# Kernel tuning notes

Measured on AMD Instinct MI355X. Metric: run time of the kernel, lower is better.

Reference implementation:

```python
import jax, jax.numpy as jnp
import numpy as np
import math

EMB, HID, SEQ, BATCH, VOCAB, LAYERS = 512, 1024, 128, 64, 10000, 2


def setup_inputs() -> dict:
    key = jax.random.key(0)
    ks = jax.random.split(key, 8)
    bnd = math.sqrt(1.0 / HID)
    return {
        "inputs": jax.random.randint(ks[0], (SEQ, BATCH), 0, VOCAB),
        "hidden": jnp.zeros((LAYERS, BATCH, HID), jnp.float32),
        "emb": jax.random.uniform(ks[1], (VOCAB, EMB), jnp.float32, -0.1, 0.1),
        "W_x0": jax.random.uniform(ks[2], (EMB, HID), jnp.float32, -bnd, bnd),
        "W_x1": jax.random.uniform(ks[3], (HID, HID), jnp.float32, -bnd, bnd),
        "W_h": jax.random.uniform(ks[4], (LAYERS, HID, HID), jnp.float32, -bnd, bnd),
        "b_h": jax.random.uniform(ks[5], (LAYERS, HID), jnp.float32, -bnd, bnd),
        "W_out": jax.random.uniform(ks[6], (HID, VOCAB), jnp.float32, -0.1, 0.1),
        "b_out": jnp.zeros((VOCAB,), jnp.float32),
    }


def reference(inputs, hidden, emb, W_x0, W_x1, W_h, b_h, W_out, b_out):
    # Stacked vanilla RNN over time; dropout is identity (dp_keep_prob=1.0).
    scale = jnp.asarray(math.sqrt(EMB), jnp.float32)  # WordEmbedding * sqrt(n_units)

    def step(h, tok):
        # h: (L, B, H); tok: (B,)
        x = emb[tok] * scale                                   # (B, E)
        h0 = jnp.tanh(x @ W_x0 + h[0] @ W_h[0] + b_h[0])       # (B, H)
        h1 = jnp.tanh(h0 @ W_x1 + h[1] @ W_h[1] + b_h[1])      # (B, H)
        logits_t = h1 @ W_out + b_out                          # (B, V)
        return jnp.stack([h0, h1]), logits_t

    final_hidden, logits = jax.lax.scan(step, hidden, inputs)
    return logits, final_hidden
```

## Files before the change

kernel.cpp:

```cpp
#include <hip/hip_runtime.h>
#include <math.h>


typedef unsigned short u16;
typedef unsigned long long u64;
typedef __bf16 bf16x8 __attribute__((ext_vector_type(8)));
typedef float  f32x4  __attribute__((ext_vector_type(4)));
typedef unsigned int u32x4 __attribute__((ext_vector_type(4)));
typedef u16 u16x8 __attribute__((ext_vector_type(8)));

#define SEQ_ 128
#define B_   64
#define E_   512
#define H_   1024
#define V_   10000
#define VP_  10112
#define ROWS_ (SEQ_*B_)
#define BH_  (B_*H_)
#define LOGITS_ 81920000
#define NWG_ 192

__device__ __forceinline__ u16 f2bf(float f) {
  unsigned u = __builtin_bit_cast(unsigned, f);
  u += 0x7fffu + ((u >> 16) & 1u);
  return (u16)(u >> 16);
}
__device__ __forceinline__ float bf2f(u16 h) {
  unsigned u = ((unsigned)h) << 16;
  return __builtin_bit_cast(float, u);
}
__device__ __forceinline__ void st64(void* p, u64 v) {
  __hip_atomic_store((u64*)p, v, __ATOMIC_RELAXED, __HIP_MEMORY_SCOPE_AGENT);
}
__device__ __forceinline__ u64 pk64(float a, float b) {
  return (u64)__builtin_bit_cast(unsigned, a) |
         ((u64)__builtin_bit_cast(unsigned, b) << 32);
}


__global__ __launch_bounds__(256)
void transpose_split(const float* __restrict__ in, u16* __restrict__ outHi,
                     u16* __restrict__ outLo, int K, int N, int NP)
{
  __shared__ float tile[32][33];
  const int n0 = blockIdx.x * 32, k0 = blockIdx.y * 32;
  const int x = threadIdx.x & 31;
  const int y = threadIdx.x >> 5;
  (void)NP;
#pragma unroll
  for (int i = 0; i < 4; ++i) {
    const int r = y * 4 + i;
    const int n = n0 + x;
    tile[r][x] = (n < N) ? in[(size_t)(k0 + r) * N + n] : 0.f;
  }
  __syncthreads();
#pragma unroll
  for (int i = 0; i < 4; ++i) {
    const int r = y * 4 + i;
    const int n = n0 + r;
    const int k = k0 + x;
    const float v = tile[x][r];
    const u16 hb = f2bf(v);
    outHi[(size_t)n * K + k] = hb;
    if (outLo) outLo[(size_t)n * K + k] = f2bf(v - bf2f(hb));
  }
}

__global__ __launch_bounds__(256)
void gather_x(const int* __restrict__ toks, const float* __restrict__ emb,
              u16* __restrict__ XBhi, u16* __restrict__ XBlo)
{
  const int tid = blockIdx.x * 256 + threadIdx.x;
  const int row = tid >> 6;
  const int c8 = (tid & 63) * 8;
  const int tok = toks[row];
  const float* e = emb + (size_t)tok * E_ + c8;
  u16x8 hv, lv;
#pragma unroll
  for (int j = 0; j < 8; ++j) {
    float f = e[j] * 22.627416997969522f;
    u16 hb = f2bf(f);
    hv[j] = hb;
    lv[j] = f2bf(f - bf2f(hb));
  }
  *(u16x8*)(XBhi + (size_t)row * E_ + c8) = hv;
  *(u16x8*)(XBlo + (size_t)row * E_ + c8) = lv;
}

__global__ __launch_bounds__(256)
void hid_cast(const float* __restrict__ h, u16* H0hi, u16* H0lo, u16* H1hi, u16* H1lo)
{
  const int tid = blockIdx.x * 256 + threadIdx.x;
  float v0 = h[tid], v1 = h[BH_ + tid];
  u16 a = f2bf(v0); H0hi[tid] = a; H0lo[tid] = f2bf(v0 - bf2f(a));
  u16 b = f2bf(v1); H1hi[tid] = b; H1lo[tid] = f2bf(v1 - bf2f(b));
}

template<int NPASS>
__global__ __launch_bounds__(256)
void gemm_bf16(const u16* __restrict__ Ahi, const u16* __restrict__ Alo,
               const u16* __restrict__ Bhi, const u16* __restrict__ Blo,
               const float* __restrict__ bias, float* __restrict__ C,
               int K, int Nreal, int ldc, int nbx, int nby)
{
  constexpr int LDT = 40;
  __shared__ u16 lds[(NPASS == 3 ? 4 : 2) * 128 * LDT];
  u16* As  = lds;
  u16* Bs  = lds + 128 * LDT;
  u16* As2 = (NPASS == 3) ? (lds + 2 * 128 * LDT) : lds;
  u16* Bs2 = (NPASS == 3) ? (lds + 3 * 128 * LDT) : lds;

  const int S = 8;
  int bid  = blockIdx.x;
  int scol = bid / (S * nby);
  int rem  = bid - scol * (S * nby);
  int w    = nbx - scol * S; if (w > S) w = S;
  int bx   = scol * S + rem % w;
  int by   = rem / w;
  const int m0 = by * 128, n0 = bx * 128;

  const int tid  = threadIdx.x;
  const int wave = tid >> 6, lane = tid & 63;
  const int wm = (wave & 1) * 64, wn = (wave >> 1) * 64;
  const int lrow = lane & 15, lk = (lane >> 4) * 8;

  f32x4 acc[4][4] = {};

  const int kTiles = K >> 5;
  for (int kt = 0; kt < kTiles; ++kt) {
    const int k0 = kt << 5;
    __syncthreads();
#pragma unroll
    for (int c = tid; c < 512; c += 256) {
      const int row = c >> 2, kq = c & 3;
      const int l = row * LDT + kq * 8;
      *(u32x4*)(As + l) = *(const u32x4*)(Ahi + (size_t)(m0 + row) * K + k0 + kq * 8);
      *(u32x4*)(Bs + l) = *(const u32x4*)(Bhi + (size_t)(n0 + row) * K + k0 + kq * 8);
      if constexpr (NPASS == 3) {
        *(u32x4*)(As2 + l) = *(const u32x4*)(Alo + (size_t)(m0 + row) * K + k0 + kq * 8);
        *(u32x4*)(Bs2 + l) = *(const u32x4*)(Blo + (size_t)(n0 + row) * K + k0 + kq * 8);
      }
    }
    __syncthreads();
    bf16x8 a[4], b[4];
#pragma unroll
    for (int i = 0; i < 4; ++i) {
      a[i] = *(const bf16x8*)(As + (wm + i * 16 + lrow) * LDT + lk);
      b[i] = *(const bf16x8*)(Bs + (wn + i * 16 + lrow) * LDT + lk);
    }
    if constexpr (NPASS == 3) {
      bf16x8 a2[4], b2[4];
#pragma unroll
      for (int i = 0; i < 4; ++i) {
        a2[i] = *(const bf16x8*)(As2 + (wm + i * 16 + lrow) * LDT + lk);
        b2[i] = *(const bf16x8*)(Bs2 + (wn + i * 16 + lrow) * LDT + lk);
      }
#pragma unroll
      for (int mi = 0; mi < 4; ++mi)
#pragma unroll
        for (int ni = 0; ni < 4; ++ni) {
          acc[mi][ni] = __builtin_amdgcn_mfma_f32_16x16x32_bf16(a[mi],  b[ni],  acc[mi][ni], 0, 0, 0);
          acc[mi][ni] = __builtin_amdgcn_mfma_f32_16x16x32_bf16(a[mi],  b2[ni], acc[mi][ni], 0, 0, 0);
          acc[mi][ni] = __builtin_amdgcn_mfma_f32_16x16x32_bf16(a2[mi], b[ni],  acc[mi][ni], 0, 0, 0);
        }
    } else {
#pragma unroll
      for (int mi = 0; mi < 4; ++mi)
#pragma unroll
        for (int ni = 0; ni < 4; ++ni)
          acc[mi][ni] = __builtin_amdgcn_mfma_f32_16x16x32_bf16(a[mi], b[ni], acc[mi][ni], 0, 0, 0);
    }
  }
#pragma unroll
  for (int mi = 0; mi < 4; ++mi)
#pragma unroll
    for (int ni = 0; ni < 4; ++ni)
#pragma unroll
      for (int r = 0; r < 4; ++r) {
        const int row = m0 + wm + mi * 16 + (lane >> 4) * 4 + r;
        const int col = n0 + wn + ni * 16 + lrow;
        if (col < Nreal) {
          float v = acc[mi][ni][r];
          if (bias) v += bias[col];
          C[(size_t)row * ldc + col] = v;
        }
      }
}

__device__ __forceinline__ void gbar192(unsigned* flags, unsigned my)
{
  asm volatile("s_waitcnt vmcnt(0)" ::: "memory");
  __syncthreads();
  if (threadIdx.x == 0)
    __hip_atomic_store(flags + blockIdx.x * 16u, my, __ATOMIC_RELAXED,
                       __HIP_MEMORY_SCOPE_AGENT);
  if (threadIdx.x < 64) {
    const int l = threadIdx.x;
    bool ok0 = false, ok1 = false, ok2 = false;
    for (;;) {
      if (!ok0) ok0 = __hip_atomic_load(flags + l * 16,         __ATOMIC_RELAXED, __HIP_MEMORY_SCOPE_AGENT) >= my;
      if (!ok1) ok1 = __hip_atomic_load(flags + (l + 64) * 16,  __ATOMIC_RELAXED, __HIP_MEMORY_SCOPE_AGENT) >= my;
      if (!ok2) ok2 = __hip_atomic_load(flags + (l + 128) * 16, __ATOMIC_RELAXED, __HIP_MEMORY_SCOPE_AGENT) >= my;
      if (__all(ok0 && ok1 && ok2)) break;
      __builtin_amdgcn_s_sleep(2);
    }
  }
  __syncthreads();
}

__global__ __launch_bounds__(256, 1)
void recur_fused(const u16* __restrict__ Wh0h, const u16* __restrict__ Wh0l,
                 const u16* __restrict__ Wx1h, const u16* __restrict__ Wx1l,
                 const u16* __restrict__ Wh1h, const u16* __restrict__ Wh1l,
                 const float* __restrict__ XP0, const float* __restrict__ b1,
                 float* __restrict__ Pbuf,
                 u16* __restrict__ H0hi, u16* __restrict__ H0lo,
                 u16* __restrict__ H1hi, u16* __restrict__ H1lo,
                 float* __restrict__ final0, float* __restrict__ final1,
                 unsigned* __restrict__ flags)
{
  __shared__ u16 bsm[2 * 32 * 1024];

  const int wg   = blockIdx.x;
  const int role = (wg < 64) ? 0 : (wg < 128) ? 1 : 2;
  const int idx  = wg & 63;
  const int bg   = idx >> 5, cg = idx & 31;

  const u16* Bhi = (role == 0) ? Wh0h : (role == 1) ? Wx1h : Wh1h;
  const u16* Blo = (role == 0) ? Wh0l : (role == 1) ? Wx1l : Wh1l;

  const int tid  = threadIdx.x;
  const int wv   = tid >> 6, lane = tid & 63;
  const int wbg  = wv >> 1, wcg = wv & 1;
  const int lb   = lane & 15;
  const int lk8  = (lane >> 4) * 8;

  for (int c = tid; c < 8192; c += 256) {
    const int p   = c >> 12;
    const int cc  = c & 4095;
    const int col = cc >> 7;
    const int k8  = (cc & 127) * 8;
    u32x4 v = *(const u32x4*)((p ? Blo : Bhi) + (size_t)(cg * 32 + col) * H_ + k8);
    *(u32x4*)(bsm + p * 32768 + col * 1024 + (k8 ^ ((col & 7) << 3))) = v;
  }
  __syncthreads();

  const int batch = bg * 32 + wbg * 16 + lb;
  const int c0    = cg * 32 + wcg * 16 + (lk8 >> 1);
  const int colL  = wcg * 16 + lb;
  const int xorv  = (colL & 7) << 3;
  const u16* bsp  = bsm + colL * 1024;
  const size_t aoff = (size_t)batch * H_ + lk8;

  for (int i = 0; i < 130; ++i) {
    bool active; int t;
    if (role == 0)      { active = (i < 128);           t = i;     }
    else if (role == 1) { active = (i >= 1 && i < 129); t = i - 1; }
    else                { active = (i >= 2);            t = i - 2; }

    if (active) {
      const u16 *Ahi, *Alo;
      const float* initp;
      if (role == 0) {
        Ahi = H0hi + (size_t)t * BH_;  Alo = H0lo + (size_t)t * BH_;
        initp = XP0 + (size_t)t * BH_ + (size_t)batch * H_ + c0;
      } else if (role == 1) {
        Ahi = H0hi + (size_t)(t + 1) * BH_;  Alo = H0lo + (size_t)(t + 1) * BH_;
        initp = b1 + c0;
      } else {
        Ahi = H1hi + (size_t)t * BH_;  Alo = H1lo + (size_t)t * BH_;
        initp = Pbuf + (size_t)t * BH_ + (size_t)batch * H_ + c0;
      }

      f32x4 acc0 = *(const f32x4*)initp;
      f32x4 acc1 = {0.f, 0.f, 0.f, 0.f};
#pragma unroll
      for (int kc = 0; kc < 32; ++kc) {
        bf16x8 ah = *(const bf16x8*)(Ahi + aoff + kc * 32);
        bf16x8 al = *(const bf16x8*)(Alo + aoff + kc * 32);
        bf16x8 bh = *(const bf16x8*)(bsp + ((kc * 32 + lk8) ^ xorv));
        bf16x8 bl = *(const bf16x8*)(bsp + 32768 + ((kc * 32 + lk8) ^ xorv));
        if (kc & 1) {
          acc1 = __builtin_amdgcn_mfma_f32_16x16x32_bf16(bh, ah, acc1, 0, 0, 0);
          acc1 = __builtin_amdgcn_mfma_f32_16x16x32_bf16(bl, ah, acc1, 0, 0, 0);
          acc1 = __builtin_amdgcn_mfma_f32_16x16x32_bf16(bh, al, acc1, 0, 0, 0);
        } else {
          acc0 = __builtin_amdgcn_mfma_f32_16x16x32_bf16(bh, ah, acc0, 0, 0, 0);
          acc0 = __builtin_amdgcn_mfma_f32_16x16x32_bf16(bl, ah, acc0, 0, 0, 0);
          acc0 = __builtin_amdgcn_mfma_f32_16x16x32_bf16(bh, al, acc0, 0, 0, 0);
        }
      }
      acc0 = acc0 + acc1;

      if (role == 1) {
        float* op = Pbuf + (size_t)t * BH_ + (size_t)batch * H_ + c0;
        st64(op,     pk64(acc0[0], acc0[1]));
        st64(op + 2, pk64(acc0[2], acc0[3]));
      } else {
        float hv[4];
        u64 whi = 0, wlo = 0;
#pragma unroll
        for (int r = 0; r < 4; ++r) {
          float v = tanhf(acc0[r]);
          u16 hb = f2bf(v);
          u16 lo = f2bf(v - bf2f(hb));
          whi |= (u64)hb << (16 * r);
          wlo |= (u64)lo << (16 * r);
          hv[r] = v;
        }
        u16* OH = (role == 0 ? H0hi : H1hi) + (size_t)(t + 1) * BH_ + (size_t)batch * H_ + c0;
        u16* OL = (role == 0 ? H0lo : H1lo) + (size_t)(t + 1) * BH_ + (size_t)batch * H_ + c0;
        st64(OH, whi);
        st64(OL, wlo);
        if (t == SEQ_ - 1) {
          float* fp = (role == 0 ? final0 : final1) + (size_t)batch * H_ + c0;
          st64(fp,     pk64(hv[0], hv[1]));
          st64(fp + 2, pk64(hv[2], hv[3]));
        }
      }
    }
    if (i < 129) gbar192(flags, (unsigned)(i + 1));
  }
}

extern "C" void kernel_launch(void* const* d_in, const int* in_sizes, int n_in,
                              void* d_out, int out_size, void* d_ws, size_t ws_size,
                              hipStream_t stream)
{
  (void)in_sizes; (void)n_in; (void)out_size; (void)ws_size;
  const int*   toks = (const int*)d_in[0];
  const float* hid0 = (const float*)d_in[1];
  const float* emb  = (const float*)d_in[2];
  const float* Wx0  = (const float*)d_in[3];
  const float* Wx1  = (const float*)d_in[4];
  const float* Wh   = (const float*)d_in[5];
  const float* bh   = (const float*)d_in[6];
  const float* Wout = (const float*)d_in[7];
  const float* bout = (const float*)d_in[8];
  float* out = (float*)d_out;

  char* ws = (char*)d_ws;
  size_t off = 0;
  auto alloc = [&](size_t bytes) -> void* {
    void* p = ws + off;
    off += (bytes + 255) & ~(size_t)255;
    return p;
  };
  unsigned* flags = (unsigned*)alloc(16384);
  u16* XBhi  = (u16*)alloc((size_t)ROWS_ * E_ * 2);
  u16* XBlo  = (u16*)alloc((size_t)ROWS_ * E_ * 2);
  u16* Wx0Th = (u16*)alloc((size_t)H_ * E_ * 2);
  u16* Wx0Tl = (u16*)alloc((size_t)H_ * E_ * 2);
  u16* Wx1Th = (u16*)alloc((size_t)H_ * H_ * 2);
  u16* Wx1Tl = (u16*)alloc((size_t)H_ * H_ * 2);
  u16* Wh0Th = (u16*)alloc((size_t)H_ * H_ * 2);
  u16* Wh0Tl = (u16*)alloc((size_t)H_ * H_ * 2);
  u16* Wh1Th = (u16*)alloc((size_t)H_ * H_ * 2);
  u16* Wh1Tl = (u16*)alloc((size_t)H_ * H_ * 2);
  u16* WoutT = (u16*)alloc((size_t)VP_ * H_ * 2);
  float* XP0 = (float*)alloc((size_t)ROWS_ * H_ * 4);
  float* Pbuf= (float*)alloc((size_t)SEQ_ * BH_ * 4);
  u16* H0hi  = (u16*)alloc((size_t)(SEQ_ + 1) * BH_ * 2);
  u16* H0lo  = (u16*)alloc((size_t)(SEQ_ + 1) * BH_ * 2);
  u16* H1hi  = (u16*)alloc((size_t)(SEQ_ + 1) * BH_ * 2);
  u16* H1lo  = (u16*)alloc((size_t)(SEQ_ + 1) * BH_ * 2);

  hipMemsetAsync(flags, 0, 16384, stream);
  transpose_split<<<dim3(H_ / 32, E_ / 32), 256, 0, stream>>>(Wx0, Wx0Th, Wx0Tl, E_, H_, H_);
  transpose_split<<<dim3(H_ / 32, H_ / 32), 256, 0, stream>>>(Wx1, Wx1Th, Wx1Tl, H_, H_, H_);
  transpose_split<<<dim3(H_ / 32, H_ / 32), 256, 0, stream>>>(Wh,           Wh0Th, Wh0Tl, H_, H_, H_);
  transpose_split<<<dim3(H_ / 32, H_ / 32), 256, 0, stream>>>(Wh + H_ * H_, Wh1Th, Wh1Tl, H_, H_, H_);
  transpose_split<<<dim3(VP_ / 32, H_ / 32), 256, 0, stream>>>(Wout, WoutT, nullptr, H_, V_, VP_);
  gather_x<<<ROWS_ * E_ / 8 / 256, 256, 0, stream>>>(toks, emb, XBhi, XBlo);
  hid_cast<<<BH_ / 256, 256, 0, stream>>>(hid0, H0hi, H0lo, H1hi, H1lo);

  gemm_bf16<3><<<8 * 64, 256, 0, stream>>>(XBhi, XBlo, Wx0Th, Wx0Tl, bh, XP0,
                                           E_, H_, H_, 8, 64);
  recur_fused<<<NWG_, 256, 0, stream>>>(Wh0Th, Wh0Tl, Wx1Th, Wx1Tl, Wh1Th, Wh1Tl,
                                        XP0, bh + H_, Pbuf,
                                        H0hi, H0lo, H1hi, H1lo,
                                        out + LOGITS_, out + LOGITS_ + BH_, flags);
  gemm_bf16<1><<<79 * 64, 256, 0, stream>>>(H1hi + BH_, nullptr, WoutT, nullptr,
                                            bout, out, H_, V_, V_, 79, 64);
}
```

Measured before the change: 1.741 ms.

## Replace global grid barrier with per-wave dataflow flags in recurrent kernel

The single 192-workgroup barrier per step is replaced by fine-grained per-wave, per-timestep, per-batch-group flags. Each role now waits only on the specific producers it depends on: layer0 on itself, the Wx1 projection on layer0, and layer1 on itself and the projection. This lets the pipeline stages drift relative to each other and removes __syncthreads from the step loop. It also swaps tanhf for an exp/rcp-based fast tanh, which may lose some accuracy near saturation and uses a much larger flag array that must be zeroed each launch.

```diff
diff --git a/kernel.cpp b/kernel.cpp
--- a/kernel.cpp
+++ b/kernel.cpp
@@ -19,6 +19,7 @@
 #define BH_  (B_*H_)
 #define LOGITS_ 81920000
 #define NWG_ 192
+#define FPS_ (129*128)
 
 __device__ __forceinline__ u16 f2bf(float f) {
   unsigned u = __builtin_bit_cast(unsigned, f);
@@ -35,6 +36,10 @@
 __device__ __forceinline__ u64 pk64(float a, float b) {
   return (u64)__builtin_bit_cast(unsigned, a) |
          ((u64)__builtin_bit_cast(unsigned, b) << 32);
+}
+__device__ __forceinline__ float tanh_fast(float x) {
+  float e = __expf(2.0f * x);
+  return 1.0f - 2.0f * __builtin_amdgcn_rcpf(e + 1.0f);
 }
 
 
@@ -187,29 +192,51 @@
       }
 }
 
-__device__ __forceinline__ void gbar192(unsigned* flags, unsigned my)
+__device__ __forceinline__ void pollW(const unsigned* f)
+{
+  const int l = threadIdx.x & 63;
+  for (;;) {
+    unsigned a = __hip_atomic_load(f + l,      __ATOMIC_RELAXED, __HIP_MEMORY_SCOPE_AGENT);
+    unsigned b = __hip_atomic_load(f + l + 64, __ATOMIC_RELAXED, __HIP_MEMORY_SCOPE_AGENT);
+    if (__all((a != 0) & (b != 0))) break;
+    __builtin_amdgcn_s_sleep(1);
+  }
+  asm volatile("" ::: "memory");
+}
+__device__ __forceinline__ void publish(unsigned* f)
 {
   asm volatile("s_waitcnt vmcnt(0)" ::: "memory");
-  __syncthreads();
-  if (threadIdx.x == 0)
-    __hip_atomic_store(flags + blockIdx.x * 16u, my, __ATOMIC_RELAXED,
-                       __HIP_MEMORY_SCOPE_AGENT);
-  if (threadIdx.x < 64) {
-    const int l = threadIdx.x;
-    bool ok0 = false, ok1 = false, ok2 = false;
-    for (;;) {
-      if (!ok0) ok0 = __hip_atomic_load(flags + l * 16,         __ATOMIC_RELAXED, __HIP_MEMORY_SCOPE_AGENT) >= my;
-      if (!ok1) ok1 = __hip_atomic_load(flags + (l + 64) * 16,  __ATOMIC_RELAXED, __HIP_MEMORY_SCOPE_AGENT) >= my;
-      if (!ok2) ok2 = __hip_atomic_load(flags + (l + 128) * 16, __ATOMIC_RELAXED, __HIP_MEMORY_SCOPE_AGENT) >= my;
-      if (__all(ok0 && ok1 && ok2)) break;
-      __builtin_amdgcn_s_sleep(2);
-    }
-  }
-  __syncthreads();
+  if ((threadIdx.x & 63) == 0)
+    __hip_atomic_store(f, 1u, __ATOMIC_RELAXED, __HIP_MEMORY_SCOPE_AGENT);
+}
+
+__device__ __forceinline__ f32x4 gemm96(const u16* __restrict__ Ahi,
+                                        const u16* __restrict__ Alo,
+                                        const u16* bsp, int xorv, int lk8,
+                                        size_t aoff, f32x4 acc0)
+{
+  f32x4 acc1 = {0.f, 0.f, 0.f, 0.f};
+#pragma unroll
+  for (int kc = 0; kc < 32; ++kc) {
+    bf16x8 ah = *(const bf16x8*)(Ahi + aoff + kc * 32);
+    bf16x8 al = *(const bf16x8*)(Alo + aoff + kc * 32);
+    bf16x8 bh = *(const bf16x8*)(bsp + ((kc * 32 + lk8) ^ xorv));
+    bf16x8 bl = *(const bf16x8*)(bsp + 32768 + ((kc * 32 + lk8) ^ xorv));
+    if (kc & 1) {
+      acc1 = __builtin_amdgcn_mfma_f32_16x16x32_bf16(bh, ah, acc1, 0, 0, 0);
+      acc1 = __builtin_amdgcn_mfma_f32_16x16x32_bf16(bl, ah, acc1, 0, 0, 0);
+      acc1 = __builtin_amdgcn_mfma_f32_16x16x32_bf16(bh, al, acc1, 0, 0, 0);
+    } else {
+      acc0 = __builtin_amdgcn_mfma_f32_16x16x32_bf16(bh, ah, acc0, 0, 0, 0);
+      acc0 = __builtin_amdgcn_mfma_f32_16x16x32_bf16(bl, ah, acc0, 0, 0, 0);
+      acc0 = __builtin_amdgcn_mfma_f32_16x16x32_bf16(bh, al, acc0, 0, 0, 0);
+    }
+  }
+  return acc0 + acc1;
 }
 
 __global__ __launch_bounds__(256, 1)
-void recur_fused(const u16* __restrict__ Wh0h, const u16* __restrict__ Wh0l,
+void recur_roles(const u16* __restrict__ Wh0h, const u16* __restrict__ Wh0l,
                  const u16* __restrict__ Wx1h, const u16* __restrict__ Wx1l,
                  const u16* __restrict__ Wh1h, const u16* __restrict__ Wh1l,
                  const float* __restrict__ XP0, const float* __restrict__ b1,
@@ -222,7 +249,7 @@
   __shared__ u16 bsm[2 * 32 * 1024];
 
   const int wg   = blockIdx.x;
-  const int role = (wg < 64) ? 0 : (wg < 128) ? 1 : 2;
+  const int role = wg >> 6;
   const int idx  = wg & 63;
   const int bg   = idx >> 5, cg = idx & 31;
 
@@ -251,75 +278,71 @@
   const int xorv  = (colL & 7) << 3;
   const u16* bsp  = bsm + colL * 1024;
   const size_t aoff = (size_t)batch * H_ + lk8;
-
-  for (int i = 0; i < 130; ++i) {
-    bool active; int t;
-    if (role == 0)      { active = (i < 128);           t = i;     }
-    else if (role == 1) { active = (i >= 1 && i < 129); t = i - 1; }
-    else                { active = (i >= 2);            t = i - 2; }
-
-    if (active) {
-      const u16 *Ahi, *Alo;
-      const float* initp;
-      if (role == 0) {
-        Ahi = H0hi + (size_t)t * BH_;  Alo = H0lo + (size_t)t * BH_;
-        initp = XP0 + (size_t)t * BH_ + (size_t)batch * H_ + c0;
-      } else if (role == 1) {
-        Ahi = H0hi + (size_t)(t + 1) * BH_;  Alo = H0lo + (size_t)(t + 1) * BH_;
-        initp = b1 + c0;
-      } else {
-        Ahi = H1hi + (size_t)t * BH_;  Alo = H1lo + (size_t)t * BH_;
-        initp = Pbuf + (size_t)t * BH_ + (size_t)batch * H_ + c0;
-      }
-
-      f32x4 acc0 = *(const f32x4*)initp;
-      f32x4 acc1 = {0.f, 0.f, 0.f, 0.f};
-#pragma unroll
-      for (int kc = 0; kc < 32; ++kc) {
-        bf16x8 ah = *(const bf16x8*)(Ahi + aoff + kc * 32);
-        bf16x8 al = *(const bf16x8*)(Alo + aoff + kc * 32);
-        bf16x8 bh = *(const bf16x8*)(bsp + ((kc * 32 + lk8) ^ xorv));
-        bf16x8 bl = *(const bf16x8*)(bsp + 32768 + ((kc * 32 + lk8) ^ xorv));
-        if (kc & 1) {
-          acc1 = __builtin_amdgcn_mfma_f32_16x16x32_bf16(bh, ah, acc1, 0, 0, 0);
-          acc1 = __builtin_amdgcn_mfma_f32_16x16x32_bf16(bl, ah, acc1, 0, 0, 0);
-          acc1 = __builtin_amdgcn_mfma_f32_16x16x32_bf16(bh, al, acc1, 0, 0, 0);
-        } else {
-          acc0 = __builtin_amdgcn_mfma_f32_16x16x32_bf16(bh, ah, acc0, 0, 0, 0);
-          acc0 = __builtin_amdgcn_mfma_f32_16x16x32_bf16(bl, ah, acc0, 0, 0, 0);
-          acc0 = __builtin_amdgcn_mfma_f32_16x16x32_bf16(bh, al, acc0, 0, 0, 0);
-        }
-      }
-      acc0 = acc0 + acc1;
-
-      if (role == 1) {
-        float* op = Pbuf + (size_t)t * BH_ + (size_t)batch * H_ + c0;
-        st64(op,     pk64(acc0[0], acc0[1]));
-        st64(op + 2, pk64(acc0[2], acc0[3]));
-      } else {
-        float hv[4];
-        u64 whi = 0, wlo = 0;
-#pragma unroll
-        for (int r = 0; r < 4; ++r) {
-          float v = tanhf(acc0[r]);
-          u16 hb = f2bf(v);
-          u16 lo = f2bf(v - bf2f(hb));
-          whi |= (u64)hb << (16 * r);
-          wlo |= (u64)lo << (16 * r);
-          hv[r] = v;
-        }
-        u16* OH = (role == 0 ? H0hi : H1hi) + (size_t)(t + 1) * BH_ + (size_t)batch * H_ + c0;
-        u16* OL = (role == 0 ? H0lo : H1lo) + (size_t)(t + 1) * BH_ + (size_t)batch * H_ + c0;
-        st64(OH, whi);
-        st64(OL, wlo);
-        if (t == SEQ_ - 1) {
-          float* fp = (role == 0 ? final0 : final1) + (size_t)batch * H_ + c0;
-          st64(fp,     pk64(hv[0], hv[1]));
-          st64(fp + 2, pk64(hv[2], hv[3]));
-        }
-      }
-    }
-    if (i < 129) gbar192(flags, (unsigned)(i + 1));
+  const size_t boff = (size_t)batch * H_ + c0;
+
+  unsigned* flg0 = flags;
+  unsigned* flgP = flags + 2 * FPS_;
+  unsigned* flg1 = flags + 4 * FPS_;
+  const int fme  = cg * 4 + wv;
+
+  if (role == 0) {
+    for (int t = 0; t < SEQ_; ++t) {
+      f32x4 init = *(const f32x4*)(XP0 + (size_t)t * BH_ + boff);
+      if (t >= 1) pollW(flg0 + ((size_t)bg * 129 + t) * 128);
+      f32x4 acc = gemm96(H0hi + (size_t)t * BH_, H0lo + (size_t)t * BH_,
+                         bsp, xorv, lk8, aoff, init);
+      u64 whi = 0, wlo = 0; float hv[4];
+#pragma unroll
+      for (int r = 0; r < 4; ++r) {
+        float v = tanh_fast(acc[r]);
+        u16 hb = f2bf(v);
+        whi |= (u64)hb << (16 * r);
+        wlo |= (u64)f2bf(v - bf2f(hb)) << (16 * r);
+        hv[r] = v;
+      }
+      st64(H0hi + (size_t)(t + 1) * BH_ + boff, whi);
+      st64(H0lo + (size_t)(t + 1) * BH_ + boff, wlo);
+      if (t == SEQ_ - 1) {
+        st64(final0 + boff,     pk64(hv[0], hv[1]));
+        st64(final0 + boff + 2, pk64(hv[2], hv[3]));
+      }
+      publish(flg0 + ((size_t)bg * 129 + (t + 1)) * 128 + fme);
+    }
+  } else if (role == 1) {
+    const f32x4 binit = *(const f32x4*)(b1 + c0);
+    for (int s = 1; s <= SEQ_; ++s) {
+      pollW(flg0 + ((size_t)bg * 129 + s) * 128);
+      f32x4 acc = gemm96(H0hi + (size_t)s * BH_, H0lo + (size_t)s * BH_,
+                         bsp, xorv, lk8, aoff, binit);
+      float* op = Pbuf + (size_t)(s - 1) * BH_ + boff;
+      st64(op,     pk64(acc[0], acc[1]));
+      st64(op + 2, pk64(acc[2], acc[3]));
+      publish(flgP + ((size_t)bg * 129 + s) * 128 + fme);
+    }
+  } else {
+    for (int s = 1; s <= SEQ_; ++s) {
+      if (s >= 2) pollW(flg1 + ((size_t)bg * 129 + (s - 1)) * 128);
+      pollW(flgP + ((size_t)bg * 129 + s) * 128);
+      f32x4 init = *(const f32x4*)(Pbuf + (size_t)(s - 1) * BH_ + boff);
+      f32x4 acc = gemm96(H1hi + (size_t)(s - 1) * BH_, H1lo + (size_t)(s - 1) * BH_,
+                         bsp, xorv, lk8, aoff, init);
+      u64 whi = 0, wlo = 0; float hv[4];
+#pragma unroll
+      for (int r = 0; r < 4; ++r) {
+        float v = tanh_fast(acc[r]);
+        u16 hb = f2bf(v);
+        whi |= (u64)hb << (16 * r);
+        wlo |= (u64)f2bf(v - bf2f(hb)) << (16 * r);
+        hv[r] = v;
+      }
+      st64(H1hi + (size_t)s * BH_ + boff, whi);
+      st64(H1lo + (size_t)s * BH_ + boff, wlo);
+      if (s == SEQ_) {
+        st64(final1 + boff,     pk64(hv[0], hv[1]));
+        st64(final1 + boff + 2, pk64(hv[2], hv[3]));
+      }
+      publish(flg1 + ((size_t)bg * 129 + s) * 128 + fme);
+    }
   }
 }
 
@@ -346,7 +369,7 @@
     off += (bytes + 255) & ~(size_t)255;
     return p;
   };
-  unsigned* flags = (unsigned*)alloc(16384);
+  unsigned* flags = (unsigned*)alloc(6 * FPS_ * 4);
   u16* XBhi  = (u16*)alloc((size_t)ROWS_ * E_ * 2);
   u16* XBlo  = (u16*)alloc((size_t)ROWS_ * E_ * 2);
   u16* Wx0Th = (u16*)alloc((size_t)H_ * E_ * 2);
@@ -365,7 +388,7 @@
   u16* H1hi  = (u16*)alloc((size_t)(SEQ_ + 1) * BH_ * 2);
   u16* H1lo  = (u16*)alloc((size_t)(SEQ_ + 1) * BH_ * 2);
 
-  hipMemsetAsync(flags, 0, 16384, stream);
+  hipMemsetAsync(flags, 0, 6 * FPS_ * 4, stream);
   transpose_split<<<dim3(H_ / 32, E_ / 32), 256, 0, stream>>>(Wx0, Wx0Th, Wx0Tl, E_, H_, H_);
   transpose_split<<<dim3(H_ / 32, H_ / 32), 256, 0, stream>>>(Wx1, Wx1Th, Wx1Tl, H_, H_, H_);
   transpose_split<<<dim3(H_ / 32, H_ / 32), 256, 0, stream>>>(Wh,           Wh0Th, Wh0Tl, H_, H_, H_);
@@ -376,7 +399,7 @@
 
   gemm_bf16<3><<<8 * 64, 256, 0, stream>>>(XBhi, XBlo, Wx0Th, Wx0Tl, bh, XP0,
                                            E_, H_, H_, 8, 64);
-  recur_fused<<<NWG_, 256, 0, stream>>>(Wh0Th, Wh0Tl, Wx1Th, Wx1Tl, Wh1Th, Wh1Tl,
+  recur_roles<<<NWG_, 256, 0, stream>>>(Wh0Th, Wh0Tl, Wx1Th, Wx1Tl, Wh1Th, Wh1Tl,
                                         XP0, bh + H_, Pbuf,
                                         H0hi, H0lo, H1hi, H1lo,
                                         out + LOGITS_, out + LOGITS_ + BH_, flags);
```

Result: slower. 2.224 ms (+27.7%).
